# Optimization experiments

Hardware: AMD Instinct MI355X
Metric: run time of the kernel (lower is better)

Reference implementation:

```python
import jax, jax.numpy as jnp
import numpy as np

N_CODES = 512
CODE_DIM = 32
BETA = 0.25


def setup_inputs() -> dict:
    key = jax.random.key(0)
    k1, k2 = jax.random.split(key)
    z_e = jax.random.normal(k1, (8192, 64, CODE_DIM), dtype=jnp.float32)
    # codebook initialized uniform in [-1/n_codes, 1/n_codes] as in the torch module
    codebook = jax.random.uniform(
        k2, (N_CODES, CODE_DIM), dtype=jnp.float32,
        minval=-1.0 / N_CODES, maxval=1.0 / N_CODES)
    return {"z_e": z_e, "codebook": codebook}


def reference(z_e, codebook):
    # squared-distance matrix: ||z||^2 - 2 z.W^T + ||W||^2  -> [B, T, n_codes]
    dists = (jnp.sum(z_e * z_e, axis=-1, keepdims=True)
             - 2.0 * jnp.einsum('btd,nd->btn', z_e, codebook)
             + jnp.sum(codebook * codebook, axis=-1))
    indices = jnp.argmin(dists, axis=-1)          # [B, T] int
    z_q = codebook[indices]                        # [B, T, code_dim]
    sg = jax.lax.stop_gradient
    codebook_loss = jnp.mean((z_q - sg(z_e)) ** 2)
    commit_loss = jnp.mean((z_e - sg(z_q)) ** 2)
    loss = codebook_loss + BETA * commit_loss
    # straight-through estimator
    z_q_st = z_e + sg(z_q - z_e)
    return (z_q_st, indices, loss)
```

## Files before the change

### kernel.cpp

```cpp
#include <hip/hip_runtime.h>

#define N_CODES 512
#define D 32
#define NVEC (8192 * 64)
#define ZQ_ELEMS (NVEC * D)
#define NBLK (NVEC / 256)
#define MARGIN_TRIG 7e-5f
#define SA (-1.0f / 16.0f)
#define SB (32.0f)
#define KMASK5 0xFFFFFFE0u

typedef _Float16 half8 __attribute__((ext_vector_type(8)));
typedef float f32x4 __attribute__((ext_vector_type(4)));

#define WW1_OFF 2112
#define BFRAG_OFF 4160
#define WT_OFF 36928
#define PART_OFF 102464
#define WL_OFF 118848
#define STAGE_F4 2176

__device__ __forceinline__ unsigned umin_(unsigned a, unsigned b) { return a < b ? a : b; }
__device__ __forceinline__ unsigned umax_(unsigned a, unsigned b) { return a > b ? a : b; }

__global__ void vq_prep(const float* __restrict__ cb, float* __restrict__ ww,
                        float* __restrict__ ww1, half8* __restrict__ bfrag,
                        float* __restrict__ wT, unsigned* __restrict__ flagcnt) {
    int gid = blockIdx.x * 256 + threadIdx.x;
    if (gid == 0) *flagcnt = 0u;
    if (gid >= 2048) return;
    int t = gid >> 6, l = gid & 63;
    int code = t * 16 + (l & 15), koff = (l >> 4) * 8;
    const float* w = cb + (size_t)code * D + koff;
    half8 h;
#pragma unroll
    for (int j = 0; j < 8; ++j) h[j] = (_Float16)(SB * w[j]);
    bfrag[t * 64 + l] = h;
#pragma unroll
    for (int j = 0; j < 8; ++j)
        wT[(koff + j) * N_CODES + code] = w[j];
    if (koff == 0) {
        const float* wr = cb + (size_t)code * D;
        double s = 0.0;
#pragma unroll
        for (int d = 0; d < D; ++d) s = fma((double)wr[d], (double)wr[d], s);
        ww[code] = (float)s;
        ww1[code] = (float)(1.0 + s);
    }
}

__global__ __launch_bounds__(256, 4) void vq_main(
        const float* __restrict__ z, const float* __restrict__ cbf,
        const float4* __restrict__ stage_src,
        float* __restrict__ zq, float* __restrict__ idxo,
        double* __restrict__ partials, unsigned* __restrict__ flagcnt,
        int* __restrict__ worklist, int wl_cap) {
    __shared__ __align__(16) char smem[38912];
    __shared__ double wsum[4];
    const int tid = threadIdx.x;

    {
        float4* s4 = (float4*)smem;
#pragma unroll
        for (int i = 0; i < 9; ++i) {
            int k = i * 256 + tid;
            if (k < STAGE_F4) s4[k] = stage_src[k];
        }
    }
    const float* lds_cin = (const float*)smem;
    const char* lds_bf = smem + 2048;
    float4* scratch = (float4*)(smem + 34816);

    const int l = tid & 63, wv = tid >> 6;
    const int g16 = l & 15, kg = l >> 4, koff = kg * 8;
    const int vblock = blockIdx.x * 256;
    const int vwave = vblock + wv * 64;

    __syncthreads();

#pragma unroll 1
    for (int vt = 0; vt < 4; ++vt) {
        const float* zp = z + (size_t)(vwave + vt * 16 + g16) * D + koff;
        float4 a0 = *(const float4*)zp;
        float4 a1 = *(const float4*)(zp + 4);
        half8 Bz;
        Bz[0] = (_Float16)(a0.x * SA); Bz[1] = (_Float16)(a0.y * SA);
        Bz[2] = (_Float16)(a0.z * SA); Bz[3] = (_Float16)(a0.w * SA);
        Bz[4] = (_Float16)(a1.x * SA); Bz[5] = (_Float16)(a1.y * SA);
        Bz[6] = (_Float16)(a1.z * SA); Bz[7] = (_Float16)(a1.w * SA);
        float ss = 0.f;
        ss = fmaf(a0.x, a0.x, ss); ss = fmaf(a0.y, a0.y, ss);
        ss = fmaf(a0.z, a0.z, ss); ss = fmaf(a0.w, a0.w, ss);
        ss = fmaf(a1.x, a1.x, ss); ss = fmaf(a1.y, a1.y, ss);
        ss = fmaf(a1.z, a1.z, ss); ss = fmaf(a1.w, a1.w, ss);

        unsigned m1c[4], m2c[4];
#pragma unroll
        for (int r = 0; r < 4; ++r) { m1c[r] = 0xFFFFFFFFu; m2c[r] = 0xFFFFFFFFu; }

#pragma unroll
        for (int tp = 0; tp < 16; ++tp) {
            half8 W0 = *(const half8*)(lds_bf + (2 * tp) * 1024 + l * 16);
            half8 W1 = *(const half8*)(lds_bf + (2 * tp + 1) * 1024 + l * 16);
            f32x4 cv0 = *(const f32x4*)(lds_cin + (2 * tp) * 16 + kg * 4);
            f32x4 cv1 = *(const f32x4*)(lds_cin + (2 * tp + 1) * 16 + kg * 4);
            f32x4 acc0 = __builtin_amdgcn_mfma_f32_16x16x32_f16(W0, Bz, cv0, 0, 0, 0);
            f32x4 acc1 = __builtin_amdgcn_mfma_f32_16x16x32_f16(W1, Bz, cv1, 0, 0, 0);
#pragma unroll
            for (int r = 0; r < 4; ++r) {
                unsigned k0 = (__float_as_uint(acc0[r]) & KMASK5) | (unsigned)(2 * tp);
                unsigned k1 = (__float_as_uint(acc1[r]) & KMASK5) | (unsigned)(2 * tp + 1);
                unsigned med;
                asm("v_med3_u32 %0, %1, %2, %3"
                    : "=v"(med) : "v"(m1c[r]), "v"(k0), "v"(k1));
                asm("v_min3_u32 %0, %1, %2, %3"
                    : "=v"(m1c[r]) : "v"(m1c[r]), "v"(k0), "v"(k1));
                m2c[r] = umin_(m2c[r], med);
            }
        }

        unsigned a01 = umin_(m1c[0], m1c[1]), x01 = umax_(m1c[0], m1c[1]);
        unsigned a23 = umin_(m1c[2], m1c[3]), x23 = umax_(m1c[2], m1c[3]);
        unsigned b1 = umin_(a01, a23);
        unsigned sec = umin_(umax_(a01, a23), umin_(x01, x23));
        unsigned m2all = umin_(umin_(m2c[0], m2c[1]), umin_(m2c[2], m2c[3]));
        unsigned b2 = umin_(sec, m2all);
        int rwin = (m1c[0] == b1) ? 0
                 : (m1c[1] == b1) ? 1
                 : (m1c[2] == b1) ? 2 : 3;
        unsigned mymin = b1;

#pragma unroll
        for (int dd = 16; dd <= 32; dd <<= 1) {
            unsigned o1 = __shfl_xor(b1, dd, 64);
            unsigned o2 = __shfl_xor(b2, dd, 64);
            float os = __shfl_xor(ss, dd, 64);
            b2 = umin_(umin_(b2, o2), umax_(b1, o1));
            b1 = umin_(b1, o1);
            ss += os;
        }
        unsigned long long bal =
            __ballot(mymin == b1) & (0x0001000100010001ull << g16);
        int firstl = __builtin_ctzll(bal);
        int rw = __shfl(rwin, firstl, 64);
        int code = (int)(b1 & 31u) * 16 + (firstl >> 4) * 4 + rw;
        if (kg == 0)
            scratch[wv * 64 + vt * 16 + g16] =
                make_float4(__uint_as_float(b1 & KMASK5),
                            __uint_as_float(b2 & KMASK5),
                            __int_as_float(code), ss);
    }
    __syncthreads();

    float4 my = scratch[tid];
    int bai = __float_as_int(my.z);

    {
        bool flag = (my.y - my.x) <= MARGIN_TRIG;
        unsigned long long mask = __ballot(flag);
        if (mask) {
            int base = 0;
            if (l == 0) base = (int)atomicAdd(flagcnt, (unsigned)__popcll(mask));
            base = __shfl(base, 0, 64);
            if (flag) {
                int pos = base + (int)__popcll(mask & ((1ull << l) - 1ull));
                if (pos < wl_cap) worklist[pos] = vblock + tid;
            }
        }
    }

    {
        double contrib = ((double)my.x - 1.0) + (double)my.w;
#pragma unroll
        for (int off = 32; off; off >>= 1) contrib += __shfl_down(contrib, off, 64);
        if (l == 0) wsum[wv] = contrib;
    }
    __syncthreads();
    if (tid == 0) partials[blockIdx.x] = wsum[0] + wsum[1] + wsum[2] + wsum[3];

    idxo[vblock + tid] = (float)bai;

    {
        const float4* cb4 = (const float4*)cbf;
        float4* zq4 = (float4*)zq;
        const int c = tid & 7;
#pragma unroll
        for (int it = 0; it < 8; ++it) {
            int r = it * 32 + (tid >> 3);
            int win = __float_as_int(scratch[r].z);
            float4 val = cb4[(size_t)win * 8 + c];
            zq4[(size_t)(vblock + r) * 8 + c] = val;
        }
    }
}

__global__ __launch_bounds__(256, 2) void vq_fixup(
        const float* __restrict__ z, const float* __restrict__ cbf,
        const float* __restrict__ wT, const float* __restrict__ c32g,
        float* __restrict__ zq, float* __restrict__ idxo,
        const unsigned* __restrict__ flagcnt,
        const int* __restrict__ worklist, int wl_cap,
        const double* __restrict__ partials, float* __restrict__ loss_out) {
    if (blockIdx.x == 0) {
        const int tid = threadIdx.x;
        double s = 0.0;
#pragma unroll
        for (int i = 0; i < NBLK / 256; ++i) s += partials[i * 256 + tid];
#pragma unroll
        for (int off = 32; off; off >>= 1) s += __shfl_down(s, off, 64);
        __shared__ double w4[4];
        if ((tid & 63) == 0) w4[tid >> 6] = s;
        __syncthreads();
        if (tid == 0)
            *loss_out = (float)(1.25 * (w4[0] + w4[1] + w4[2] + w4[3])
                                / (double)ZQ_ELEMS);
    }

    int cnt = (int)*flagcnt; if (cnt > wl_cap) cnt = wl_cap;
    const int l = threadIdx.x & 63;
    const int wave = (blockIdx.x * blockDim.x + threadIdx.x) >> 6;
    const int nwaves = (gridDim.x * blockDim.x) >> 6;

    for (int e = wave; e < cnt; e += nwaves) {
        int v = worklist[e];
        const float* zv = z + (size_t)v * D;
        float zd[D];
#pragma unroll
        for (int q = 0; q < 8; ++q) {
            float4 t = *(const float4*)(zv + q * 4);
            zd[4 * q + 0] = t.x; zd[4 * q + 1] = t.y;
            zd[4 * q + 2] = t.z; zd[4 * q + 3] = t.w;
        }
        double Ad = 0.0;
#pragma unroll
        for (int d = 0; d < D; ++d) Ad = fma((double)zd[d], (double)zd[d], Ad);
        float Af = (float)Ad;

        double bd[8];
#pragma unroll
        for (int k = 0; k < 8; ++k) bd[k] = 0.0;
#pragma unroll 4
        for (int d = 0; d < D; ++d) {
            double zdd = (double)zd[d];
            const float* wrow = wT + (size_t)d * N_CODES + l;
#pragma unroll
            for (int k = 0; k < 8; ++k)
                bd[k] = fma(zdd, (double)wrow[64 * k], bd[k]);
        }
        float best = 1e30f; int bi = 0;
#pragma unroll
        for (int k = 0; k < 8; ++k) {
            int c = l + 64 * k;
            float B32 = (float)bd[k];
            float dq = __fadd_rn(__fsub_rn(Af, __fmul_rn(2.0f, B32)), c32g[c]);
            if (dq < best) { best = dq; bi = c; }
        }
#pragma unroll
        for (int dd = 1; dd < 64; dd <<= 1) {
            float ob = __shfl_xor(best, dd, 64);
            int obi = __shfl_xor(bi, dd, 64);
            bool take = (ob < best) || (ob == best && obi < bi);
            best = take ? ob : best; bi = take ? obi : bi;
        }
        if (l == 0) idxo[v] = (float)bi;
        if (l < 8) {
            float4 val = ((const float4*)cbf)[(size_t)bi * 8 + l];
            ((float4*)zq)[(size_t)v * 8 + l] = val;
        }
    }
}

extern "C" void kernel_launch(void* const* d_in, const int* in_sizes, int n_in,
                              void* d_out, int out_size, void* d_ws, size_t ws_size,
                              hipStream_t stream) {
    const float* z  = (const float*)d_in[0];
    const float* cb = (const float*)d_in[1];
    float* out  = (float*)d_out;
    float* zq   = out;
    float* idxo = out + ZQ_ELEMS;
    float* loss = out + ZQ_ELEMS + NVEC;
    unsigned* flagcnt = (unsigned*)((char*)d_ws + 8);
    float*  ww   = (float*)((char*)d_ws + 64);
    float*  ww1  = (float*)((char*)d_ws + WW1_OFF);
    half8*  bfrag = (half8*)((char*)d_ws + BFRAG_OFF);
    float*  wT   = (float*)((char*)d_ws + WT_OFF);
    const float4* stage_src = (const float4*)((char*)d_ws + WW1_OFF);
    double* partials = (double*)((char*)d_ws + PART_OFF);
    int*    worklist = (int*)((char*)d_ws + WL_OFF);
    long long avail = (long long)ws_size - WL_OFF;
    int wl_cap = avail > 0 ? (int)(avail / 4 < NVEC ? avail / 4 : NVEC) : 0;

    vq_prep<<<8, 256, 0, stream>>>(cb, ww, ww1, bfrag, wT, flagcnt);
    vq_main<<<NBLK, 256, 0, stream>>>(z, cb, stage_src, zq, idxo,
                                      partials, flagcnt, worklist, wl_cap);
    vq_fixup<<<1024, 256, 0, stream>>>(z, cb, wT, ww, zq, idxo,
                                       flagcnt, worklist, wl_cap, partials, loss);
}
```

Measured before the change: 124.2 us.

## Stage transposed codebook in LDS for fixup and coalesce its transpose in prep

```diff
diff --git a/kernel.cpp b/kernel.cpp
--- a/kernel.cpp
+++ b/kernel.cpp
@@ -28,24 +28,32 @@
                         float* __restrict__ wT, unsigned* __restrict__ flagcnt) {
     int gid = blockIdx.x * 256 + threadIdx.x;
     if (gid == 0) *flagcnt = 0u;
-    if (gid >= 2048) return;
-    int t = gid >> 6, l = gid & 63;
-    int code = t * 16 + (l & 15), koff = (l >> 4) * 8;
-    const float* w = cb + (size_t)code * D + koff;
-    half8 h;
-#pragma unroll
-    for (int j = 0; j < 8; ++j) h[j] = (_Float16)(SB * w[j]);
-    bfrag[t * 64 + l] = h;
-#pragma unroll
-    for (int j = 0; j < 8; ++j)
-        wT[(koff + j) * N_CODES + code] = w[j];
-    if (koff == 0) {
-        const float* wr = cb + (size_t)code * D;
+    {
+        int flat = gid * 4;
+        int d = flat >> 9, c = flat & 511;
+        float4 v;
+        v.x = cb[(size_t)(c + 0) * D + d];
+        v.y = cb[(size_t)(c + 1) * D + d];
+        v.z = cb[(size_t)(c + 2) * D + d];
+        v.w = cb[(size_t)(c + 3) * D + d];
+        *(float4*)(wT + flat) = v;
+    }
+    if (gid < 2048) {
+        int t = gid >> 6, l = gid & 63;
+        int code = t * 16 + (l & 15), koff = (l >> 4) * 8;
+        const float* w = cb + (size_t)code * D + koff;
+        half8 h;
+#pragma unroll
+        for (int j = 0; j < 8; ++j) h[j] = (_Float16)(SB * w[j]);
+        bfrag[t * 64 + l] = h;
+    }
+    if (gid < N_CODES) {
+        const float* wr = cb + (size_t)gid * D;
         double s = 0.0;
 #pragma unroll
         for (int d = 0; d < D; ++d) s = fma((double)wr[d], (double)wr[d], s);
-        ww[code] = (float)s;
-        ww1[code] = (float)(1.0 + s);
+        ww[gid] = (float)s;
+        ww1[gid] = (float)(1.0 + s);
     }
 }
 
@@ -194,32 +202,41 @@
     }
 }
 
-__global__ __launch_bounds__(256, 2) void vq_fixup(
+__global__ __launch_bounds__(512, 2) void vq_fixup(
         const float* __restrict__ z, const float* __restrict__ cbf,
         const float* __restrict__ wT, const float* __restrict__ c32g,
         float* __restrict__ zq, float* __restrict__ idxo,
         const unsigned* __restrict__ flagcnt,
         const int* __restrict__ worklist, int wl_cap,
         const double* __restrict__ partials, float* __restrict__ loss_out) {
-    if (blockIdx.x == 0) {
-        const int tid = threadIdx.x;
+    __shared__ __align__(16) float wl_lds[D * N_CODES];
+    __shared__ double w4[4];
+    const int tid = threadIdx.x;
+
+    {
+        float4* s4 = (float4*)wl_lds;
+        const float4* g4 = (const float4*)wT;
+#pragma unroll
+        for (int i = 0; i < 8; ++i) s4[i * 512 + tid] = g4[i * 512 + tid];
+    }
+
+    if (blockIdx.x == 0 && tid < 256) {
         double s = 0.0;
 #pragma unroll
         for (int i = 0; i < NBLK / 256; ++i) s += partials[i * 256 + tid];
 #pragma unroll
         for (int off = 32; off; off >>= 1) s += __shfl_down(s, off, 64);
-        __shared__ double w4[4];
         if ((tid & 63) == 0) w4[tid >> 6] = s;
-        __syncthreads();
-        if (tid == 0)
-            *loss_out = (float)(1.25 * (w4[0] + w4[1] + w4[2] + w4[3])
-                                / (double)ZQ_ELEMS);
-    }
+    }
+    __syncthreads();
+    if (blockIdx.x == 0 && tid == 0)
+        *loss_out = (float)(1.25 * (w4[0] + w4[1] + w4[2] + w4[3])
+                            / (double)ZQ_ELEMS);
 
     int cnt = (int)*flagcnt; if (cnt > wl_cap) cnt = wl_cap;
-    const int l = threadIdx.x & 63;
-    const int wave = (blockIdx.x * blockDim.x + threadIdx.x) >> 6;
-    const int nwaves = (gridDim.x * blockDim.x) >> 6;
+    const int l = tid & 63;
+    const int wave = (blockIdx.x * 512 + tid) >> 6;
+    const int nwaves = (gridDim.x * 512) >> 6;
 
     for (int e = wave; e < cnt; e += nwaves) {
         int v = worklist[e];
@@ -242,7 +259,7 @@
 #pragma unroll 4
         for (int d = 0; d < D; ++d) {
             double zdd = (double)zd[d];
-            const float* wrow = wT + (size_t)d * N_CODES + l;
+            const float* wrow = wl_lds + d * N_CODES + l;
 #pragma unroll
             for (int k = 0; k < 8; ++k)
                 bd[k] = fma(zdd, (double)wrow[64 * k], bd[k]);
@@ -290,9 +307,9 @@
     long long avail = (long long)ws_size - WL_OFF;
     int wl_cap = avail > 0 ? (int)(avail / 4 < NVEC ? avail / 4 : NVEC) : 0;
 
-    vq_prep<<<8, 256, 0, stream>>>(cb, ww, ww1, bfrag, wT, flagcnt);
+    vq_prep<<<16, 256, 0, stream>>>(cb, ww, ww1, bfrag, wT, flagcnt);
     vq_main<<<NBLK, 256, 0, stream>>>(z, cb, stage_src, zq, idxo,
                                       partials, flagcnt, worklist, wl_cap);
-    vq_fixup<<<1024, 256, 0, stream>>>(z, cb, wT, ww, zq, idxo,
-                                       flagcnt, worklist, wl_cap, partials, loss);
+    vq_fixup<<<512, 512, 0, stream>>>(z, cb, wT, ww, zq, idxo,
+                                      flagcnt, worklist, wl_cap, partials, loss);
 }
```

Measured after the change: 117.9 us. -5.1%, faster.
